# Optimization experiments

Measured on AMD Instinct MI355X. Metric: run time of the kernel, lower is better.

## Reference

```python
import jax, jax.numpy as jnp
import numpy as np

MUL = 32            # multiplicity of each irrep
N_NODES = 16384
N_EDGES = 262144
AVG_NEIGH = 16.0
N_SPECIES = 4
RADIAL_DIM = 8
INV_SQRT3 = 0.5773502691896258  # normalized CG coeff for 1o x 1o -> 0e (dot)


def setup_inputs() -> dict:
    key = jax.random.key(0)
    ks = jax.random.split(key, 14)
    f32 = jnp.float32
    return {
        "node_features": jax.random.normal(ks[0], (N_NODES, 4 * MUL), dtype=f32),
        "edge_sh": jax.random.normal(ks[1], (N_EDGES, 4), dtype=f32),
        "radial_embedding": jax.random.uniform(ks[2], (N_EDGES, RADIAL_DIM), dtype=f32),
        "W_up_s": jax.random.normal(ks[3], (MUL, MUL), dtype=f32),
        "W_up_v": jax.random.normal(ks[4], (MUL, MUL), dtype=f32),
        "W_r1": jax.random.normal(ks[5], (RADIAL_DIM, RADIAL_DIM), dtype=f32),
        "W_r2": jax.random.normal(ks[6], (RADIAL_DIM, 4 * MUL), dtype=f32),
        "W_dn_s": jax.random.normal(ks[7], (2 * MUL, 2 * MUL), dtype=f32),
        "W_dn_v": jax.random.normal(ks[8], (2 * MUL, MUL), dtype=f32),
        "W_sk_s": jax.random.normal(ks[9], (N_SPECIES, MUL, 2 * MUL), dtype=f32),
        "W_sk_v": jax.random.normal(ks[10], (N_SPECIES, MUL, MUL), dtype=f32),
        "senders": jax.random.randint(ks[11], (N_EDGES,), 0, N_NODES),
        "receivers": jax.random.randint(ks[12], (N_EDGES,), 0, N_NODES),
        "node_species": jax.random.randint(ks[13], (N_NODES,), 0, N_SPECIES),
    }


def reference(node_features, edge_sh, radial_embedding, W_up_s, W_up_v,
              W_r1, W_r2, W_dn_s, W_dn_v, W_sk_s, W_sk_v,
              senders, receivers, node_species):
    n = node_features.shape[0]
    # irreps layout: 32x0e (first MUL cols) + 32x1o (next 3*MUL cols)
    s = node_features[:, :MUL]                      # [N, mul]     0e
    v = node_features[:, MUL:].reshape(n, MUL, 3)   # [N, mul, 3]  1o

    # linear_up: per-irrep channel mixing, 1/sqrt(fan_in) normalization
    s1 = (s @ W_up_s) * (MUL ** -0.5)
    v1 = jnp.einsum('nmi,mk->nki', v, W_up_v) * (MUL ** -0.5)

    # gather sender features per edge
    ss = s1[senders]              # [E, mul]
    vs = v1[senders]              # [E, mul, 3]
    yv = edge_sh[:, 1:4]          # 1o part of edge spherical harmonics (0e part dropped in TP)

    # Clebsch-Gordan tensor product, filtered to output irreps {0e, 1o}:
    #   0e x 1o -> 1o ;  1o x 1o -> 0e (dot, coeff 1/sqrt(3)); cross(1e) & 2e dropped
    m_v_tp = ss[:, :, None] * yv[:, None, :]                 # [E, mul, 3]
    m_s_tp = jnp.einsum('emi,ei->em', vs, yv) * INV_SQRT3    # [E, mul]

    # radial MLP -> one scalar weight per irrep instance of the message
    h = jax.nn.silu((radial_embedding @ W_r1) * (RADIAL_DIM ** -0.5))
    w = (h @ W_r2) * (RADIAL_DIM ** -0.5)                    # [E, 4*mul]
    w_ss, w_vs, w_vt, w_st = jnp.split(w, 4, axis=1)

    # message = concat(self-features, tensor-product paths), radially weighted
    m_s = jnp.concatenate([ss * w_ss, m_s_tp * w_st], axis=1)                          # [E, 2*mul]
    m_v = jnp.concatenate([vs * w_vs[:, :, None], m_v_tp * w_vt[:, :, None]], axis=1)  # [E, 2*mul, 3]

    # scatter-add into receiver nodes, divide by sqrt(avg_num_neighbours)
    inv = AVG_NEIGH ** -0.5
    S = jax.ops.segment_sum(m_s, receivers, num_segments=n) * inv                     # [N, 2*mul]
    V = jax.ops.segment_sum(m_v.reshape(m_v.shape[0], -1), receivers,
                            num_segments=n).reshape(n, 2 * MUL, 3) * inv              # [N, 2*mul, 3]

    # linear_down to gate irreps: MUL 0e features + MUL gate scalars, MUL 1o vectors
    g_s = (S @ W_dn_s) * ((2 * MUL) ** -0.5)                                          # [N, 2*mul]
    g_v = jnp.einsum('nmi,mk->nki', V, W_dn_v) * ((2 * MUL) ** -0.5)                  # [N, mul, 3]

    # species-indexed skip connection from the original node features
    sk_s = jnp.einsum('nm,nmk->nk', s, W_sk_s[node_species]) * (MUL ** -0.5)
    sk_v = jnp.einsum('nmi,nmk->nki', v, W_sk_v[node_species]) * (MUL ** -0.5)
    g_s = 0.5 * (g_s + sk_s)
    g_v = 0.5 * (g_v + sk_v)

    # gate nonlinearity: silu on even scalars, silu(gates) multiplies each 1o vector
    feat_s = jax.nn.silu(g_s[:, :MUL])
    gates = jax.nn.silu(g_s[:, MUL:])
    out_v = g_v * gates[:, :, None]
    return jnp.concatenate([feat_s, out_v.reshape(n, 3 * MUL)], axis=1)  # [N, 4*mul]
```

## Files before the change

### kernel.cpp

```cpp
#include <hip/hip_runtime.h>
#include <hip/hip_bf16.h>
#include <hip/hip_fp16.h>

#define N_NODES 16384
#define N_EDGES 262144
#define MUL 32
#define REC_CAP (N_EDGES + 3 * N_NODES + 16)

#if defined(__has_builtin)
#if __has_builtin(__builtin_amdgcn_fdot2)
#define HAS_FDOT2 1
#endif
#endif

typedef _Float16 h2_t __attribute__((ext_vector_type(2)));

__device__ __forceinline__ float silu_f(float x) {
    return x / (1.0f + __expf(-x));
}
__device__ __forceinline__ __half2 i2h2(int v) { return __builtin_bit_cast(__half2, v); }
__device__ __forceinline__ int h22i(__half2 v) { return __builtin_bit_cast(int, v); }
__device__ __forceinline__ h2_t mkh2(float a, float b) {
    h2_t r; r[0] = (_Float16)a; r[1] = (_Float16)b; return r;
}
__device__ __forceinline__ float dot2(int hbits, h2_t w, float acc) {
#ifdef HAS_FDOT2
    return __builtin_amdgcn_fdot2(__builtin_bit_cast(h2_t, hbits), w, acc, false);
#else
    float2 h = __half22float2(i2h2(hbits));
    return acc + h.x * (float)w[0] + h.y * (float)w[1];
#endif
}

__global__ void k_up(const float* __restrict__ nf,
                     const float* __restrict__ Wus,
                     const float* __restrict__ Wuv,
                     __half* __restrict__ up_h,
                     const int* __restrict__ recv,
                     int* __restrict__ counts,
                     int* __restrict__ rank) {
    __shared__ float sh[2][128];
    int node0 = blockIdx.x * 2;
    int t = threadIdx.x;
    if (t < 32) {
        int e = blockIdx.x * 32 + t;
        rank[e] = atomicAdd(&counts[recv[e]], 1);
    }
    sh[t >> 7][t & 127] = nf[(size_t)node0 * 128 + t];
    __syncthreads();
    int local = t >> 7;
    int c = t & 127;
    int m = c >> 2, comp = c & 3;
    const float* row = sh[local];
    float acc = 0.f;
    if (comp == 0) {
        #pragma unroll
        for (int k = 0; k < 32; ++k) acc += row[k] * Wus[k * 32 + m];
    } else {
        int i = comp - 1;
        #pragma unroll
        for (int k = 0; k < 32; ++k) acc += row[32 + k * 3 + i] * Wuv[k * 32 + m];
    }
    up_h[(size_t)(node0 + local) * 128 + c] = __float2half(acc * 0.17677669529663687f);
}

__global__ void k_scan(const int* __restrict__ counts,
                       int* __restrict__ starts,
                       const float* __restrict__ Wdns,
                       const float* __restrict__ Wdnv,
                       const float* __restrict__ Wsks,
                       const float* __restrict__ Wskv,
                       float4* __restrict__ pk_dn,
                       float4* __restrict__ pk_sk) {
    __shared__ int wtot[16];
    __shared__ int woff[16];
    int t = threadIdx.x;
    int lane = t & 63, wid = t >> 6;
    const int4* cp = (const int4*)(counts + t * 16);
    int4 c0 = cp[0], c1 = cp[1], c2 = cp[2], c3 = cp[3];
    int cs[16] = {c0.x,c0.y,c0.z,c0.w,c1.x,c1.y,c1.z,c1.w,
                  c2.x,c2.y,c2.z,c2.w,c3.x,c3.y,c3.z,c3.w};
    int mysum = 0;
    #pragma unroll
    for (int i = 0; i < 16; ++i) {
        cs[i] = (cs[i] + 3) & ~3;
        mysum += cs[i];
    }
    int incl = mysum;
    #pragma unroll
    for (int off = 1; off < 64; off <<= 1) {
        int y = __shfl_up(incl, off, 64);
        if (lane >= off) incl += y;
    }
    if (lane == 63) wtot[wid] = incl;

    for (int i = t; i < 2048; i += 1024) {
        int mm = i >> 5, m = i & 31;
        pk_dn[i] = make_float4(Wdns[mm * 64 + m], Wdns[mm * 64 + 32 + m],
                               Wdnv[mm * 32 + m], 0.f);
    }
    for (int i = t; i < 4096; i += 1024) {
        int sp = i >> 10, mm = (i >> 5) & 31, m = i & 31;
        pk_sk[i] = make_float4(Wsks[sp * 2048 + mm * 64 + m],
                               Wsks[sp * 2048 + mm * 64 + 32 + m],
                               Wskv[sp * 1024 + mm * 32 + m], 0.f);
    }

    __syncthreads();
    if (t == 0) {
        int run = 0;
        #pragma unroll
        for (int w = 0; w < 16; ++w) { woff[w] = run; run += wtot[w]; }
    }
    __syncthreads();
    int run = woff[wid] + (incl - mysum);
    #pragma unroll
    for (int i = 0; i < 16; ++i) {
        starts[t * 16 + i] = run;
        run += cs[i];
    }
    if (t == 1023) starts[N_NODES] = run;
}

__global__ void k_edges(const float* __restrict__ rad,
                        const float* __restrict__ Wr1,
                        const int* __restrict__ recv,
                        const int* __restrict__ senders,
                        const float* __restrict__ esh,
                        const int* __restrict__ starts,
                        const int* __restrict__ counts,
                        const int* __restrict__ rank,
                        int4* __restrict__ records) {
    int e = blockIdx.x * blockDim.x + threadIdx.x;
    const int4 z = make_int4(0, 0, 0, 0);

    if (e < N_NODES) {
        int st = starts[e] + counts[e];
        int en = starts[e + 1];
        for (int p = st; p < en; ++p) {
            records[2 * (size_t)p] = z;
            records[2 * (size_t)p + 1] = z;
        }
    }
    if (e < 16) {
        int total = starts[N_NODES];
        records[2 * (size_t)(total + e)] = z;
        records[2 * (size_t)(total + e) + 1] = z;
    }

    const float4* rp = (const float4*)(rad + (size_t)e * 8);
    float4 a = rp[0], b = rp[1];
    float r[8] = {a.x, a.y, a.z, a.w, b.x, b.y, b.z, b.w};
    float h[8];
    #pragma unroll
    for (int j = 0; j < 8; ++j) {
        float acc = 0.f;
        #pragma unroll
        for (int k = 0; k < 8; ++k) acc += r[k] * Wr1[k * 8 + j];
        h[j] = silu_f(acc * 0.35355339059327373f);
    }
    float4 ey = *(const float4*)(esh + (size_t)e * 4);
    int snd = senders[e];
    int rc = recv[e];
    int pos = starts[rc] + rank[e];
    int4 meta;
    meta.x = snd;
    meta.y = h22i(__floats2half2_rn(ey.y, ey.z));
    meta.z = h22i(__floats2half2_rn(ey.w, 0.f));
    meta.w = 0;
    int4 hp;
    hp.x = h22i(__floats2half2_rn(h[0], h[1]));
    hp.y = h22i(__floats2half2_rn(h[2], h[3]));
    hp.z = h22i(__floats2half2_rn(h[4], h[5]));
    hp.w = h22i(__floats2half2_rn(h[6], h[7]));
    records[2 * (size_t)pos] = meta;
    records[2 * (size_t)pos + 1] = hp;
}

struct Acc {
    float S0, S1, Vv0, Vv1, Vv2, Vt0, Vt1, Vt2;
};
__device__ __forceinline__ void edge_accum(int4 meta, int4 hp, int2 q,
                                           const h2_t* __restrict__ w2a,
                                           const h2_t* __restrict__ w2b,
                                           const h2_t* __restrict__ w2c,
                                           const h2_t* __restrict__ w2d,
                                           Acc& A) {
    float wss = dot2(hp.x, w2a[0], dot2(hp.y, w2a[1], dot2(hp.z, w2a[2], dot2(hp.w, w2a[3], 0.f))));
    float wvs = dot2(hp.x, w2b[0], dot2(hp.y, w2b[1], dot2(hp.z, w2b[2], dot2(hp.w, w2b[3], 0.f))));
    float wvt = dot2(hp.x, w2c[0], dot2(hp.y, w2c[1], dot2(hp.z, w2c[2], dot2(hp.w, w2c[3], 0.f))));
    float wst = dot2(hp.x, w2d[0], dot2(hp.y, w2d[1], dot2(hp.z, w2d[2], dot2(hp.w, w2d[3], 0.f))));

    float2 y01 = __half22float2(i2h2(meta.y));
    float2 y2p = __half22float2(i2h2(meta.z));
    float y0 = y01.x, y1 = y01.y, y2 = y2p.x;
    float2 sv0 = __half22float2(i2h2(q.x));
    float2 v12 = __half22float2(i2h2(q.y));
    float ss = sv0.x, v0 = sv0.y, v1v = v12.x, v2 = v12.y;
    float dot = v0 * y0 + v1v * y1 + v2 * y2;
    A.S0 += ss * wss;
    A.S1 += dot * wst;
    A.Vv0 += v0 * wvs; A.Vv1 += v1v * wvs; A.Vv2 += v2 * wvs;
    float tv = ss * wvt;
    A.Vt0 += tv * y0; A.Vt1 += tv * y1; A.Vt2 += tv * y2;
}

__launch_bounds__(256, 4)
__global__ void k_gather(const __half* __restrict__ up_h,
                         const float* __restrict__ nf,
                         const int4* __restrict__ records,
                         const float* __restrict__ Wr2,
                         const int* __restrict__ starts,
                         const float4* __restrict__ pk_dn,
                         const float4* __restrict__ pk_sk,
                         const int* __restrict__ species,
                         float* __restrict__ out) {
    __shared__ float4 agg4[4][64];
    __shared__ float4 sk4[4][32];

    int tid = threadIdx.x;
    int w = tid >> 6;
    int lane = tid & 63;
    int sub = lane >> 5;
    int m = lane & 31;
    int node = blockIdx.x * 4 + w;

    int s0 = starts[node], s1 = starts[node + 1];

    int ta = s0 + sub;
    const int4* rp;
    rp = records + 2 * (size_t)ta;        int4 c0 = rp[0], c1 = rp[1];
    rp = records + 2 * (size_t)(ta + 2);  int4 d0 = rp[0], d1 = rp[1];

    if (lane < 32) {
        const float* src = nf + (size_t)node * 128;
        float s = src[lane];
        float a0 = src[32 + 3 * lane + 0];
        float a1 = src[32 + 3 * lane + 1];
        float a2 = src[32 + 3 * lane + 2];
        sk4[w][lane] = make_float4(s, a0, a1, a2);
    }

    int2 qa = *(const int2*)(up_h + (size_t)c0.x * 128 + m * 4);
    int2 qb = *(const int2*)(up_h + (size_t)d0.x * 128 + m * 4);

    rp = records + 2 * (size_t)(ta + 4);  int4 n0 = rp[0], n1 = rp[1];
    rp = records + 2 * (size_t)(ta + 6);  int4 e0 = rp[0], e1 = rp[1];

    const float s8 = 0.35355339059327373f;
    const float s8s3 = 0.35355339059327373f * 0.5773502691896258f;
    h2_t w2a[4], w2b[4], w2c[4], w2d[4];
    #pragma unroll
    for (int j4 = 0; j4 < 4; ++j4) {
        int j = 2 * j4;
        w2a[j4] = mkh2(Wr2[j * 128 + m] * s8,        Wr2[(j + 1) * 128 + m] * s8);
        w2b[j4] = mkh2(Wr2[j * 128 + 32 + m] * s8,   Wr2[(j + 1) * 128 + 32 + m] * s8);
        w2c[j4] = mkh2(Wr2[j * 128 + 64 + m] * s8,   Wr2[(j + 1) * 128 + 64 + m] * s8);
        w2d[j4] = mkh2(Wr2[j * 128 + 96 + m] * s8s3, Wr2[(j + 1) * 128 + 96 + m] * s8s3);
    }

    Acc A = {0.f,0.f,0.f,0.f,0.f,0.f,0.f,0.f};
    Acc B = {0.f,0.f,0.f,0.f,0.f,0.f,0.f,0.f};

    #pragma unroll 1
    for (int t0 = s0; t0 < s1; t0 += 4) {
        int2 qna = *(const int2*)(up_h + (size_t)n0.x * 128 + m * 4);
        int2 qnb = *(const int2*)(up_h + (size_t)e0.x * 128 + m * 4);

        int t2 = t0 + 8 + sub;
        rp = records + 2 * (size_t)t2;        int4 p0 = rp[0], p1 = rp[1];
        rp = records + 2 * (size_t)(t2 + 2);  int4 r0 = rp[0], r1 = rp[1];

        edge_accum(c0, c1, qa, w2a, w2b, w2c, w2d, A);
        edge_accum(d0, d1, qb, w2a, w2b, w2c, w2d, B);

        c0 = n0; c1 = n1; d0 = e0; d1 = e1;
        qa = qna; qb = qnb;
        n0 = p0; n1 = p1; e0 = r0; e1 = r1;
    }

    float accS0 = A.S0 + B.S0, accS1 = A.S1 + B.S1;
    float accVv0 = A.Vv0 + B.Vv0, accVv1 = A.Vv1 + B.Vv1, accVv2 = A.Vv2 + B.Vv2;
    float accVt0 = A.Vt0 + B.Vt0, accVt1 = A.Vt1 + B.Vt1, accVt2 = A.Vt2 + B.Vt2;

    accS0 += __shfl_xor(accS0, 32, 64);
    accS1 += __shfl_xor(accS1, 32, 64);
    accVv0 += __shfl_xor(accVv0, 32, 64);
    accVv1 += __shfl_xor(accVv1, 32, 64);
    accVv2 += __shfl_xor(accVv2, 32, 64);
    accVt0 += __shfl_xor(accVt0, 32, 64);
    accVt1 += __shfl_xor(accVt1, 32, 64);
    accVt2 += __shfl_xor(accVt2, 32, 64);

    const float inv_neigh = 0.25f;
    if (sub == 0) {
        agg4[w][m]      = make_float4(accS0 * inv_neigh, accVv0 * inv_neigh,
                                      accVv1 * inv_neigh, accVv2 * inv_neigh);
        agg4[w][32 + m] = make_float4(accS1 * inv_neigh, accVt0 * inv_neigh,
                                      accVt1 * inv_neigh, accVt2 * inv_neigh);
    }

    int sp = species[node];

    float gsa = 0.f, gsb = 0.f, gv0 = 0.f, gv1 = 0.f, gv2 = 0.f;
    {
        const float4* agp = agg4[w];
        int mm0 = sub * 32;
        #pragma unroll 4
        for (int k = 0; k < 32; ++k) {
            int mm = mm0 + k;
            float4 sv = agp[mm];
            float4 wq = pk_dn[mm * 32 + m];
            gsa += sv.x * wq.x;
            gsb += sv.x * wq.y;
            gv0 += sv.y * wq.z;
            gv1 += sv.z * wq.z;
            gv2 += sv.w * wq.z;
        }
    }
    float ska = 0.f, skb = 0.f, skv0 = 0.f, skv1 = 0.f, skv2 = 0.f;
    {
        const float4* pks = pk_sk + (size_t)sp * 1024;
        int mm0 = sub * 16;
        #pragma unroll 4
        for (int k = 0; k < 16; ++k) {
            int mm = mm0 + k;
            float4 sv = sk4[w][mm];
            float4 wq = pks[mm * 32 + m];
            ska += sv.x * wq.x;
            skb += sv.x * wq.y;
            skv0 += sv.y * wq.z;
            skv1 += sv.z * wq.z;
            skv2 += sv.w * wq.z;
        }
    }
    gsa += __shfl_xor(gsa, 32, 64);
    gsb += __shfl_xor(gsb, 32, 64);
    gv0 += __shfl_xor(gv0, 32, 64);
    gv1 += __shfl_xor(gv1, 32, 64);
    gv2 += __shfl_xor(gv2, 32, 64);
    ska += __shfl_xor(ska, 32, 64);
    skb += __shfl_xor(skb, 32, 64);
    skv0 += __shfl_xor(skv0, 32, 64);
    skv1 += __shfl_xor(skv1, 32, 64);
    skv2 += __shfl_xor(skv2, 32, 64);

    if (sub == 0) {
        const float inv8 = 0.125f;
        const float isq32 = 0.17677669529663687f;
        float a  = 0.5f * (gsa * inv8 + ska * isq32);
        float b  = 0.5f * (gsb * inv8 + skb * isq32);
        float o0 = 0.5f * (gv0 * inv8 + skv0 * isq32);
        float o1 = 0.5f * (gv1 * inv8 + skv1 * isq32);
        float o2 = 0.5f * (gv2 * inv8 + skv2 * isq32);

        float feat = silu_f(a);
        float gate = silu_f(b);
        float* o = out + (size_t)node * 128;
        o[m] = feat;
        o[32 + 3 * m + 0] = o0 * gate;
        o[32 + 3 * m + 1] = o1 * gate;
        o[32 + 3 * m + 2] = o2 * gate;
    }
}

extern "C" void kernel_launch(void* const* d_in, const int* in_sizes, int n_in,
                              void* d_out, int out_size, void* d_ws, size_t ws_size,
                              hipStream_t stream) {
    const float* nf   = (const float*)d_in[0];
    const float* esh  = (const float*)d_in[1];
    const float* rad  = (const float*)d_in[2];
    const float* Wus  = (const float*)d_in[3];
    const float* Wuv  = (const float*)d_in[4];
    const float* Wr1  = (const float*)d_in[5];
    const float* Wr2  = (const float*)d_in[6];
    const float* Wdns = (const float*)d_in[7];
    const float* Wdnv = (const float*)d_in[8];
    const float* Wsks = (const float*)d_in[9];
    const float* Wskv = (const float*)d_in[10];
    const int* senders   = (const int*)d_in[11];
    const int* receivers = (const int*)d_in[12];
    const int* species   = (const int*)d_in[13];
    float* out = (float*)d_out;

    char* ws = (char*)d_ws;
    __half* up_h   = (__half*)(ws);
    int4* records  = (int4*)(ws + (4u << 20));
    int* counts    = (int*)(ws + (14u << 20));
    int* starts    = (int*)(ws + (14u << 20) + 65536);
    int* rank      = (int*)(ws + (15u << 20));
    float4* pk_dn  = (float4*)(ws + (16u << 20));
    float4* pk_sk  = (float4*)(ws + (16u << 20) + 32768);

    hipMemsetAsync(counts, 0, 65536, stream);
    k_up<<<N_NODES / 2, 256, 0, stream>>>(nf, Wus, Wuv, up_h, receivers, counts, rank);
    k_scan<<<1, 1024, 0, stream>>>(counts, starts, Wdns, Wdnv, Wsks, Wskv, pk_dn, pk_sk);
    k_edges<<<N_EDGES / 256, 256, 0, stream>>>(rad, Wr1, receivers, senders, esh,
                                               starts, counts, rank, records);
    k_gather<<<N_NODES / 4, 256, 0, stream>>>(up_h, nf, records, Wr2, starts,
                                              pk_dn, pk_sk, species, out);
}
```

Before: 176.1 us.

## Compute edge records in edge order and scatter only indices into CSR

Edge records (radial MLP hidden, packed spherical harmonics, sender) are now computed in k_up and stored in edge order. The sorting pass only scatters 4-byte edge indices instead of 32-byte records, and padding slots point to a zeroed sentinel record. Weight packing moves from the single-block scan kernel into the scatter kernel to shorten the serial scan. The gather kernel now reads records through an extra level of indirection with random access, which adds latency and loses the sequential record reads it had before.

```diff
diff --git a/kernel.cpp b/kernel.cpp
--- a/kernel.cpp
+++ b/kernel.cpp
@@ -5,7 +5,7 @@
 #define N_NODES 16384
 #define N_EDGES 262144
 #define MUL 32
-#define REC_CAP (N_EDGES + 3 * N_NODES + 16)
+#define IDX_CAP (N_EDGES + 3 * N_NODES + 16)
 
 #if defined(__has_builtin)
 #if __has_builtin(__builtin_amdgcn_fdot2)
@@ -37,14 +37,49 @@
                      const float* __restrict__ Wuv,
                      __half* __restrict__ up_h,
                      const int* __restrict__ recv,
+                     const int* __restrict__ senders,
+                     const float* __restrict__ esh,
+                     const float* __restrict__ rad,
+                     const float* __restrict__ Wr1,
                      int* __restrict__ counts,
-                     int* __restrict__ rank) {
+                     int* __restrict__ rank,
+                     int4* __restrict__ rec_e) {
     __shared__ float sh[2][128];
     int node0 = blockIdx.x * 2;
     int t = threadIdx.x;
     if (t < 32) {
         int e = blockIdx.x * 32 + t;
-        rank[e] = atomicAdd(&counts[recv[e]], 1);
+        int rc = recv[e];
+        rank[e] = atomicAdd(&counts[rc], 1);
+        const float4* rp4 = (const float4*)(rad + (size_t)e * 8);
+        float4 a = rp4[0], b = rp4[1];
+        float r[8] = {a.x, a.y, a.z, a.w, b.x, b.y, b.z, b.w};
+        float h[8];
+        #pragma unroll
+        for (int j = 0; j < 8; ++j) {
+            float acc = 0.f;
+            #pragma unroll
+            for (int k = 0; k < 8; ++k) acc += r[k] * Wr1[k * 8 + j];
+            h[j] = silu_f(acc * 0.35355339059327373f);
+        }
+        float4 ey = *(const float4*)(esh + (size_t)e * 4);
+        int4 meta;
+        meta.x = senders[e];
+        meta.y = h22i(__floats2half2_rn(ey.y, ey.z));
+        meta.z = h22i(__floats2half2_rn(ey.w, 0.f));
+        meta.w = 0;
+        int4 hp;
+        hp.x = h22i(__floats2half2_rn(h[0], h[1]));
+        hp.y = h22i(__floats2half2_rn(h[2], h[3]));
+        hp.z = h22i(__floats2half2_rn(h[4], h[5]));
+        hp.w = h22i(__floats2half2_rn(h[6], h[7]));
+        rec_e[2 * (size_t)e] = meta;
+        rec_e[2 * (size_t)e + 1] = hp;
+    }
+    if (blockIdx.x == 0 && t == 32) {
+        const int4 z = make_int4(0, 0, 0, 0);
+        rec_e[2 * (size_t)N_EDGES] = z;
+        rec_e[2 * (size_t)N_EDGES + 1] = z;
     }
     sh[t >> 7][t & 127] = nf[(size_t)node0 * 128 + t];
     __syncthreads();
@@ -65,13 +100,7 @@
 }
 
 __global__ void k_scan(const int* __restrict__ counts,
-                       int* __restrict__ starts,
-                       const float* __restrict__ Wdns,
-                       const float* __restrict__ Wdnv,
-                       const float* __restrict__ Wsks,
-                       const float* __restrict__ Wskv,
-                       float4* __restrict__ pk_dn,
-                       float4* __restrict__ pk_sk) {
+                       int* __restrict__ starts) {
     __shared__ int wtot[16];
     __shared__ int woff[16];
     int t = threadIdx.x;
@@ -93,19 +122,6 @@
         if (lane >= off) incl += y;
     }
     if (lane == 63) wtot[wid] = incl;
-
-    for (int i = t; i < 2048; i += 1024) {
-        int mm = i >> 5, m = i & 31;
-        pk_dn[i] = make_float4(Wdns[mm * 64 + m], Wdns[mm * 64 + 32 + m],
-                               Wdnv[mm * 32 + m], 0.f);
-    }
-    for (int i = t; i < 4096; i += 1024) {
-        int sp = i >> 10, mm = (i >> 5) & 31, m = i & 31;
-        pk_sk[i] = make_float4(Wsks[sp * 2048 + mm * 64 + m],
-                               Wsks[sp * 2048 + mm * 64 + 32 + m],
-                               Wskv[sp * 1024 + mm * 32 + m], 0.f);
-    }
-
     __syncthreads();
     if (t == 0) {
         int run = 0;
@@ -122,59 +138,40 @@
     if (t == 1023) starts[N_NODES] = run;
 }
 
-__global__ void k_edges(const float* __restrict__ rad,
-                        const float* __restrict__ Wr1,
-                        const int* __restrict__ recv,
-                        const int* __restrict__ senders,
-                        const float* __restrict__ esh,
-                        const int* __restrict__ starts,
-                        const int* __restrict__ counts,
-                        const int* __restrict__ rank,
-                        int4* __restrict__ records) {
+__global__ void k_scatter(const int* __restrict__ recv,
+                          const int* __restrict__ starts,
+                          const int* __restrict__ counts,
+                          const int* __restrict__ rank,
+                          int* __restrict__ edge_idx,
+                          const float* __restrict__ Wdns,
+                          const float* __restrict__ Wdnv,
+                          const float* __restrict__ Wsks,
+                          const float* __restrict__ Wskv,
+                          float4* __restrict__ pk_dn,
+                          float4* __restrict__ pk_sk) {
     int e = blockIdx.x * blockDim.x + threadIdx.x;
-    const int4 z = make_int4(0, 0, 0, 0);
+
+    if (e < 2048) {
+        int mm = e >> 5, m = e & 31;
+        pk_dn[e] = make_float4(Wdns[mm * 64 + m], Wdns[mm * 64 + 32 + m],
+                               Wdnv[mm * 32 + m], 0.f);
+    } else if (e < 2048 + 4096) {
+        int j = e - 2048;
+        int sp = j >> 10, mm = (j >> 5) & 31, m = j & 31;
+        pk_sk[j] = make_float4(Wsks[sp * 2048 + mm * 64 + m],
+                               Wsks[sp * 2048 + mm * 64 + 32 + m],
+                               Wskv[sp * 1024 + mm * 32 + m], 0.f);
+    }
 
     if (e < N_NODES) {
         int st = starts[e] + counts[e];
         int en = starts[e + 1];
-        for (int p = st; p < en; ++p) {
-            records[2 * (size_t)p] = z;
-            records[2 * (size_t)p + 1] = z;
-        }
-    }
-    if (e < 16) {
-        int total = starts[N_NODES];
-        records[2 * (size_t)(total + e)] = z;
-        records[2 * (size_t)(total + e) + 1] = z;
-    }
-
-    const float4* rp = (const float4*)(rad + (size_t)e * 8);
-    float4 a = rp[0], b = rp[1];
-    float r[8] = {a.x, a.y, a.z, a.w, b.x, b.y, b.z, b.w};
-    float h[8];
-    #pragma unroll
-    for (int j = 0; j < 8; ++j) {
-        float acc = 0.f;
-        #pragma unroll
-        for (int k = 0; k < 8; ++k) acc += r[k] * Wr1[k * 8 + j];
-        h[j] = silu_f(acc * 0.35355339059327373f);
-    }
-    float4 ey = *(const float4*)(esh + (size_t)e * 4);
-    int snd = senders[e];
-    int rc = recv[e];
-    int pos = starts[rc] + rank[e];
-    int4 meta;
-    meta.x = snd;
-    meta.y = h22i(__floats2half2_rn(ey.y, ey.z));
-    meta.z = h22i(__floats2half2_rn(ey.w, 0.f));
-    meta.w = 0;
-    int4 hp;
-    hp.x = h22i(__floats2half2_rn(h[0], h[1]));
-    hp.y = h22i(__floats2half2_rn(h[2], h[3]));
-    hp.z = h22i(__floats2half2_rn(h[4], h[5]));
-    hp.w = h22i(__floats2half2_rn(h[6], h[7]));
-    records[2 * (size_t)pos] = meta;
-    records[2 * (size_t)pos + 1] = hp;
+        for (int p = st; p < en; ++p) edge_idx[p] = N_EDGES;
+    }
+    if (e < 16) edge_idx[starts[N_NODES] + e] = N_EDGES;
+
+    int pos = starts[recv[e]] + rank[e];
+    edge_idx[pos] = e;
 }
 
 struct Acc {
@@ -208,7 +205,8 @@
 __launch_bounds__(256, 4)
 __global__ void k_gather(const __half* __restrict__ up_h,
                          const float* __restrict__ nf,
-                         const int4* __restrict__ records,
+                         const int* __restrict__ edge_idx,
+                         const int4* __restrict__ rec_e,
                          const float* __restrict__ Wr2,
                          const int* __restrict__ starts,
                          const float4* __restrict__ pk_dn,
@@ -226,11 +224,11 @@
     int node = blockIdx.x * 4 + w;
 
     int s0 = starts[node], s1 = starts[node + 1];
-
-    int ta = s0 + sub;
-    const int4* rp;
-    rp = records + 2 * (size_t)ta;        int4 c0 = rp[0], c1 = rp[1];
-    rp = records + 2 * (size_t)(ta + 2);  int4 d0 = rp[0], d1 = rp[1];
+    int base = s0 + 2 * sub;
+
+    int2 eid0 = *(const int2*)(edge_idx + base);
+    int2 eid1 = *(const int2*)(edge_idx + base + 4);
+    int2 eid2 = *(const int2*)(edge_idx + base + 8);
 
     if (lane < 32) {
         const float* src = nf + (size_t)node * 128;
@@ -241,11 +239,14 @@
         sk4[w][lane] = make_float4(s, a0, a1, a2);
     }
 
-    int2 qa = *(const int2*)(up_h + (size_t)c0.x * 128 + m * 4);
-    int2 qb = *(const int2*)(up_h + (size_t)d0.x * 128 + m * 4);
-
-    rp = records + 2 * (size_t)(ta + 4);  int4 n0 = rp[0], n1 = rp[1];
-    rp = records + 2 * (size_t)(ta + 6);  int4 e0 = rp[0], e1 = rp[1];
+    const int4* rp;
+    rp = rec_e + 2 * (size_t)eid0.x;  int4 ca0 = rp[0], ca1 = rp[1];
+    rp = rec_e + 2 * (size_t)eid0.y;  int4 cb0 = rp[0], cb1 = rp[1];
+    rp = rec_e + 2 * (size_t)eid1.x;  int4 na0 = rp[0], na1 = rp[1];
+    rp = rec_e + 2 * (size_t)eid1.y;  int4 nb0 = rp[0], nb1 = rp[1];
+
+    int2 qa = *(const int2*)(up_h + (size_t)ca0.x * 128 + m * 4);
+    int2 qb = *(const int2*)(up_h + (size_t)cb0.x * 128 + m * 4);
 
     const float s8 = 0.35355339059327373f;
     const float s8s3 = 0.35355339059327373f * 0.5773502691896258f;
@@ -263,20 +264,22 @@
     Acc B = {0.f,0.f,0.f,0.f,0.f,0.f,0.f,0.f};
 
     #pragma unroll 1
-    for (int t0 = s0; t0 < s1; t0 += 4) {
-        int2 qna = *(const int2*)(up_h + (size_t)n0.x * 128 + m * 4);
-        int2 qnb = *(const int2*)(up_h + (size_t)e0.x * 128 + m * 4);
-
-        int t2 = t0 + 8 + sub;
-        rp = records + 2 * (size_t)t2;        int4 p0 = rp[0], p1 = rp[1];
-        rp = records + 2 * (size_t)(t2 + 2);  int4 r0 = rp[0], r1 = rp[1];
-
-        edge_accum(c0, c1, qa, w2a, w2b, w2c, w2d, A);
-        edge_accum(d0, d1, qb, w2a, w2b, w2c, w2d, B);
-
-        c0 = n0; c1 = n1; d0 = e0; d1 = e1;
+    for (int t0 = s0; t0 < s1; t0 += 4, base += 4) {
+        int2 qna = *(const int2*)(up_h + (size_t)na0.x * 128 + m * 4);
+        int2 qnb = *(const int2*)(up_h + (size_t)nb0.x * 128 + m * 4);
+
+        rp = rec_e + 2 * (size_t)eid2.x;  int4 pa0 = rp[0], pa1 = rp[1];
+        rp = rec_e + 2 * (size_t)eid2.y;  int4 pb0 = rp[0], pb1 = rp[1];
+
+        int2 eid3 = *(const int2*)(edge_idx + base + 12);
+
+        edge_accum(ca0, ca1, qa, w2a, w2b, w2c, w2d, A);
+        edge_accum(cb0, cb1, qb, w2a, w2b, w2c, w2d, B);
+
+        ca0 = na0; ca1 = na1; cb0 = nb0; cb1 = nb1;
+        na0 = pa0; na1 = pa1; nb0 = pb0; nb1 = pb1;
         qa = qna; qb = qnb;
-        n0 = p0; n1 = p1; e0 = r0; e1 = r1;
+        eid2 = eid3;
     }
 
     float accS0 = A.S0 + B.S0, accS1 = A.S1 + B.S1;
@@ -385,18 +388,21 @@
 
     char* ws = (char*)d_ws;
     __half* up_h   = (__half*)(ws);
-    int4* records  = (int4*)(ws + (4u << 20));
-    int* counts    = (int*)(ws + (14u << 20));
-    int* starts    = (int*)(ws + (14u << 20) + 65536);
-    int* rank      = (int*)(ws + (15u << 20));
-    float4* pk_dn  = (float4*)(ws + (16u << 20));
-    float4* pk_sk  = (float4*)(ws + (16u << 20) + 32768);
+    int4* rec_e    = (int4*)(ws + (4u << 20));
+    int* edge_idx  = (int*)(ws + (13u << 20));
+    int* counts    = (int*)(ws + (15u << 20));
+    int* starts    = (int*)(ws + (15u << 20) + 65536);
+    int* rank      = (int*)(ws + (15u << 20) + 131076);
+    float4* pk_dn  = (float4*)(ws + (17u << 20));
+    float4* pk_sk  = (float4*)(ws + (17u << 20) + 32768);
 
     hipMemsetAsync(counts, 0, 65536, stream);
-    k_up<<<N_NODES / 2, 256, 0, stream>>>(nf, Wus, Wuv, up_h, receivers, counts, rank);
-    k_scan<<<1, 1024, 0, stream>>>(counts, starts, Wdns, Wdnv, Wsks, Wskv, pk_dn, pk_sk);
-    k_edges<<<N_EDGES / 256, 256, 0, stream>>>(rad, Wr1, receivers, senders, esh,
-                                               starts, counts, rank, records);
-    k_gather<<<N_NODES / 4, 256, 0, stream>>>(up_h, nf, records, Wr2, starts,
+    k_up<<<N_NODES / 2, 256, 0, stream>>>(nf, Wus, Wuv, up_h, receivers, senders,
+                                          esh, rad, Wr1, counts, rank, rec_e);
+    k_scan<<<1, 1024, 0, stream>>>(counts, starts);
+    k_scatter<<<N_EDGES / 256, 256, 0, stream>>>(receivers, starts, counts, rank,
+                                                 edge_idx, Wdns, Wdnv, Wsks, Wskv,
+                                                 pk_dn, pk_sk);
+    k_gather<<<N_NODES / 4, 256, 0, stream>>>(up_h, nf, edge_idx, rec_e, Wr2, starts,
                                               pk_dn, pk_sk, species, out);
 }
```

Result: no change. 176.9 us (+0.4%).

## Fuse all stages into one cooperative persistent kernel with grid syncs

Applied to the files above, without the earlier changes.

Replaces the memset plus four kernel launches with a single cooperative kernel that runs counting, linear_up, scan, record building and the gather/output stages, separated by grid-wide syncs. Each block now owns a contiguous slice of nodes and edges and loops over them. The aim is to remove launch gaps and the serial single-block scan launch. In exchange it adds grid-sync barriers, and the scan still runs on one block of 256 threads while the rest of the grid waits. Occupancy is also limited to a grid sized for cooperative residency.

```diff
diff --git a/kernel.cpp b/kernel.cpp
--- a/kernel.cpp
+++ b/kernel.cpp
@@ -1,10 +1,11 @@
 #include <hip/hip_runtime.h>
-#include <hip/hip_bf16.h>
 #include <hip/hip_fp16.h>
+#include <hip/hip_cooperative_groups.h>
+
+namespace cg = cooperative_groups;
 
 #define N_NODES 16384
 #define N_EDGES 262144
-#define MUL 32
 #define REC_CAP (N_EDGES + 3 * N_NODES + 16)
 
 #if defined(__has_builtin)
@@ -30,151 +31,6 @@
     float2 h = __half22float2(i2h2(hbits));
     return acc + h.x * (float)w[0] + h.y * (float)w[1];
 #endif
-}
-
-__global__ void k_up(const float* __restrict__ nf,
-                     const float* __restrict__ Wus,
-                     const float* __restrict__ Wuv,
-                     __half* __restrict__ up_h,
-                     const int* __restrict__ recv,
-                     int* __restrict__ counts,
-                     int* __restrict__ rank) {
-    __shared__ float sh[2][128];
-    int node0 = blockIdx.x * 2;
-    int t = threadIdx.x;
-    if (t < 32) {
-        int e = blockIdx.x * 32 + t;
-        rank[e] = atomicAdd(&counts[recv[e]], 1);
-    }
-    sh[t >> 7][t & 127] = nf[(size_t)node0 * 128 + t];
-    __syncthreads();
-    int local = t >> 7;
-    int c = t & 127;
-    int m = c >> 2, comp = c & 3;
-    const float* row = sh[local];
-    float acc = 0.f;
-    if (comp == 0) {
-        #pragma unroll
-        for (int k = 0; k < 32; ++k) acc += row[k] * Wus[k * 32 + m];
-    } else {
-        int i = comp - 1;
-        #pragma unroll
-        for (int k = 0; k < 32; ++k) acc += row[32 + k * 3 + i] * Wuv[k * 32 + m];
-    }
-    up_h[(size_t)(node0 + local) * 128 + c] = __float2half(acc * 0.17677669529663687f);
-}
-
-__global__ void k_scan(const int* __restrict__ counts,
-                       int* __restrict__ starts,
-                       const float* __restrict__ Wdns,
-                       const float* __restrict__ Wdnv,
-                       const float* __restrict__ Wsks,
-                       const float* __restrict__ Wskv,
-                       float4* __restrict__ pk_dn,
-                       float4* __restrict__ pk_sk) {
-    __shared__ int wtot[16];
-    __shared__ int woff[16];
-    int t = threadIdx.x;
-    int lane = t & 63, wid = t >> 6;
-    const int4* cp = (const int4*)(counts + t * 16);
-    int4 c0 = cp[0], c1 = cp[1], c2 = cp[2], c3 = cp[3];
-    int cs[16] = {c0.x,c0.y,c0.z,c0.w,c1.x,c1.y,c1.z,c1.w,
-                  c2.x,c2.y,c2.z,c2.w,c3.x,c3.y,c3.z,c3.w};
-    int mysum = 0;
-    #pragma unroll
-    for (int i = 0; i < 16; ++i) {
-        cs[i] = (cs[i] + 3) & ~3;
-        mysum += cs[i];
-    }
-    int incl = mysum;
-    #pragma unroll
-    for (int off = 1; off < 64; off <<= 1) {
-        int y = __shfl_up(incl, off, 64);
-        if (lane >= off) incl += y;
-    }
-    if (lane == 63) wtot[wid] = incl;
-
-    for (int i = t; i < 2048; i += 1024) {
-        int mm = i >> 5, m = i & 31;
-        pk_dn[i] = make_float4(Wdns[mm * 64 + m], Wdns[mm * 64 + 32 + m],
-                               Wdnv[mm * 32 + m], 0.f);
-    }
-    for (int i = t; i < 4096; i += 1024) {
-        int sp = i >> 10, mm = (i >> 5) & 31, m = i & 31;
-        pk_sk[i] = make_float4(Wsks[sp * 2048 + mm * 64 + m],
-                               Wsks[sp * 2048 + mm * 64 + 32 + m],
-                               Wskv[sp * 1024 + mm * 32 + m], 0.f);
-    }
-
-    __syncthreads();
-    if (t == 0) {
-        int run = 0;
-        #pragma unroll
-        for (int w = 0; w < 16; ++w) { woff[w] = run; run += wtot[w]; }
-    }
-    __syncthreads();
-    int run = woff[wid] + (incl - mysum);
-    #pragma unroll
-    for (int i = 0; i < 16; ++i) {
-        starts[t * 16 + i] = run;
-        run += cs[i];
-    }
-    if (t == 1023) starts[N_NODES] = run;
-}
-
-__global__ void k_edges(const float* __restrict__ rad,
-                        const float* __restrict__ Wr1,
-                        const int* __restrict__ recv,
-                        const int* __restrict__ senders,
-                        const float* __restrict__ esh,
-                        const int* __restrict__ starts,
-                        const int* __restrict__ counts,
-                        const int* __restrict__ rank,
-                        int4* __restrict__ records) {
-    int e = blockIdx.x * blockDim.x + threadIdx.x;
-    const int4 z = make_int4(0, 0, 0, 0);
-
-    if (e < N_NODES) {
-        int st = starts[e] + counts[e];
-        int en = starts[e + 1];
-        for (int p = st; p < en; ++p) {
-            records[2 * (size_t)p] = z;
-            records[2 * (size_t)p + 1] = z;
-        }
-    }
-    if (e < 16) {
-        int total = starts[N_NODES];
-        records[2 * (size_t)(total + e)] = z;
-        records[2 * (size_t)(total + e) + 1] = z;
-    }
-
-    const float4* rp = (const float4*)(rad + (size_t)e * 8);
-    float4 a = rp[0], b = rp[1];
-    float r[8] = {a.x, a.y, a.z, a.w, b.x, b.y, b.z, b.w};
-    float h[8];
-    #pragma unroll
-    for (int j = 0; j < 8; ++j) {
-        float acc = 0.f;
-        #pragma unroll
-        for (int k = 0; k < 8; ++k) acc += r[k] * Wr1[k * 8 + j];
-        h[j] = silu_f(acc * 0.35355339059327373f);
-    }
-    float4 ey = *(const float4*)(esh + (size_t)e * 4);
-    int snd = senders[e];
-    int rc = recv[e];
-    int pos = starts[rc] + rank[e];
-    int4 meta;
-    meta.x = snd;
-    meta.y = h22i(__floats2half2_rn(ey.y, ey.z));
-    meta.z = h22i(__floats2half2_rn(ey.w, 0.f));
-    meta.w = 0;
-    int4 hp;
-    hp.x = h22i(__floats2half2_rn(h[0], h[1]));
-    hp.y = h22i(__floats2half2_rn(h[2], h[3]));
-    hp.z = h22i(__floats2half2_rn(h[4], h[5]));
-    hp.w = h22i(__floats2half2_rn(h[6], h[7]));
-    records[2 * (size_t)pos] = meta;
-    records[2 * (size_t)pos + 1] = hp;
 }
 
 struct Acc {
@@ -206,46 +62,152 @@
 }
 
 __launch_bounds__(256, 4)
-__global__ void k_gather(const __half* __restrict__ up_h,
-                         const float* __restrict__ nf,
-                         const int4* __restrict__ records,
-                         const float* __restrict__ Wr2,
-                         const int* __restrict__ starts,
-                         const float4* __restrict__ pk_dn,
-                         const float4* __restrict__ pk_sk,
-                         const int* __restrict__ species,
-                         float* __restrict__ out) {
+__global__ void mega(const float* __restrict__ nf, const float* __restrict__ esh,
+                     const float* __restrict__ rad, const float* __restrict__ Wus,
+                     const float* __restrict__ Wuv, const float* __restrict__ Wr1,
+                     const float* __restrict__ Wr2, const float* __restrict__ Wdns,
+                     const float* __restrict__ Wdnv, const float* __restrict__ Wsks,
+                     const float* __restrict__ Wskv, const int* __restrict__ senders,
+                     const int* __restrict__ recv, const int* __restrict__ species,
+                     float* __restrict__ out, __half* __restrict__ up_h,
+                     int4* __restrict__ records, int* __restrict__ counts,
+                     int* __restrict__ starts, int* __restrict__ rank,
+                     float4* __restrict__ pk_dn, float4* __restrict__ pk_sk) {
+    cg::grid_group gg = cg::this_grid();
+    const int b = blockIdx.x, t = threadIdx.x;
+    const int nblocks = gridDim.x;
+    const int nb = N_NODES / nblocks;
+    const int eb = N_EDGES / nblocks;
+
+    __shared__ float sh[2][128];
     __shared__ float4 agg4[4][64];
     __shared__ float4 sk4[4][32];
-
-    int tid = threadIdx.x;
-    int w = tid >> 6;
-    int lane = tid & 63;
-    int sub = lane >> 5;
-    int m = lane & 31;
-    int node = blockIdx.x * 4 + w;
-
-    int s0 = starts[node], s1 = starts[node + 1];
-
-    int ta = s0 + sub;
-    const int4* rp;
-    rp = records + 2 * (size_t)ta;        int4 c0 = rp[0], c1 = rp[1];
-    rp = records + 2 * (size_t)(ta + 2);  int4 d0 = rp[0], d1 = rp[1];
-
-    if (lane < 32) {
-        const float* src = nf + (size_t)node * 128;
-        float s = src[lane];
-        float a0 = src[32 + 3 * lane + 0];
-        float a1 = src[32 + 3 * lane + 1];
-        float a2 = src[32 + 3 * lane + 2];
-        sk4[w][lane] = make_float4(s, a0, a1, a2);
-    }
-
-    int2 qa = *(const int2*)(up_h + (size_t)c0.x * 128 + m * 4);
-    int2 qb = *(const int2*)(up_h + (size_t)d0.x * 128 + m * 4);
-
-    rp = records + 2 * (size_t)(ta + 4);  int4 n0 = rp[0], n1 = rp[1];
-    rp = records + 2 * (size_t)(ta + 6);  int4 e0 = rp[0], e1 = rp[1];
+    __shared__ int wtot[4];
+    __shared__ int woff[4];
+
+    if (t < nb) counts[b * nb + t] = 0;
+    {
+        int gid = b * 256 + t;
+        if (gid < 2048) {
+            int mm = gid >> 5, m0 = gid & 31;
+            pk_dn[gid] = make_float4(Wdns[mm * 64 + m0], Wdns[mm * 64 + 32 + m0],
+                                     Wdnv[mm * 32 + m0], 0.f);
+        } else if (gid < 6144) {
+            int j = gid - 2048;
+            int sp = j >> 10, mm = (j >> 5) & 31, m0 = j & 31;
+            pk_sk[j] = make_float4(Wsks[sp * 2048 + mm * 64 + m0],
+                                   Wsks[sp * 2048 + mm * 64 + 32 + m0],
+                                   Wskv[sp * 1024 + mm * 32 + m0], 0.f);
+        }
+    }
+    gg.sync();
+
+    for (int k = 0; k < eb; k += 256) {
+        int e = b * eb + k + t;
+        rank[e] = atomicAdd(&counts[recv[e]], 1);
+    }
+    for (int it = 0; it < nb / 2; ++it) {
+        int node0 = b * nb + it * 2;
+        sh[t >> 7][t & 127] = nf[(size_t)node0 * 128 + t];
+        __syncthreads();
+        int local = t >> 7, c = t & 127, mq = c >> 2, comp = c & 3;
+        const float* row = sh[local];
+        float acc = 0.f;
+        if (comp == 0) {
+            #pragma unroll
+            for (int k2 = 0; k2 < 32; ++k2) acc += row[k2] * Wus[k2 * 32 + mq];
+        } else {
+            int i = comp - 1;
+            #pragma unroll
+            for (int k2 = 0; k2 < 32; ++k2) acc += row[32 + k2 * 3 + i] * Wuv[k2 * 32 + mq];
+        }
+        up_h[(size_t)(node0 + local) * 128 + c] = __float2half(acc * 0.17677669529663687f);
+        __syncthreads();
+    }
+    gg.sync();
+
+    if (b == 0) {
+        int base = t * 64;
+        int tot = 0;
+        for (int i = 0; i < 64; i += 4) {
+            int4 c4 = *(const int4*)(counts + base + i);
+            tot += ((c4.x + 3) & ~3) + ((c4.y + 3) & ~3) +
+                   ((c4.z + 3) & ~3) + ((c4.w + 3) & ~3);
+        }
+        int lane2 = t & 63, wid = t >> 6;
+        int incl = tot;
+        #pragma unroll
+        for (int off = 1; off < 64; off <<= 1) {
+            int y = __shfl_up(incl, off, 64);
+            if (lane2 >= off) incl += y;
+        }
+        if (lane2 == 63) wtot[wid] = incl;
+        __syncthreads();
+        if (t == 0) {
+            int run = 0;
+            #pragma unroll
+            for (int q = 0; q < 4; ++q) { woff[q] = run; run += wtot[q]; }
+        }
+        __syncthreads();
+        int run = woff[wid] + (incl - tot);
+        for (int i = 0; i < 64; i += 4) {
+            int4 c4 = *(const int4*)(counts + base + i);
+            starts[base + i]     = run; run += (c4.x + 3) & ~3;
+            starts[base + i + 1] = run; run += (c4.y + 3) & ~3;
+            starts[base + i + 2] = run; run += (c4.z + 3) & ~3;
+            starts[base + i + 3] = run; run += (c4.w + 3) & ~3;
+        }
+        if (t == 255) starts[N_NODES] = run;
+    }
+    gg.sync();
+
+    if (t < nb) {
+        int n = b * nb + t;
+        int st = starts[n] + counts[n];
+        int en = starts[n + 1];
+        const int4 z = make_int4(0, 0, 0, 0);
+        for (int p = st; p < en; ++p) {
+            records[2 * (size_t)p] = z;
+            records[2 * (size_t)p + 1] = z;
+        }
+    }
+    if (b == 0 && t < 16) {
+        const int4 z = make_int4(0, 0, 0, 0);
+        int total = starts[N_NODES];
+        records[2 * (size_t)(total + t)] = z;
+        records[2 * (size_t)(total + t) + 1] = z;
+    }
+    for (int k = 0; k < eb; k += 256) {
+        int e = b * eb + k + t;
+        const float4* rp4 = (const float4*)(rad + (size_t)e * 8);
+        float4 a4 = rp4[0], b4 = rp4[1];
+        float r[8] = {a4.x, a4.y, a4.z, a4.w, b4.x, b4.y, b4.z, b4.w};
+        float h[8];
+        #pragma unroll
+        for (int j = 0; j < 8; ++j) {
+            float acc = 0.f;
+            #pragma unroll
+            for (int k2 = 0; k2 < 8; ++k2) acc += r[k2] * Wr1[k2 * 8 + j];
+            h[j] = silu_f(acc * 0.35355339059327373f);
+        }
+        float4 ey = *(const float4*)(esh + (size_t)e * 4);
+        int pos = starts[recv[e]] + rank[e];
+        int4 meta;
+        meta.x = senders[e];
+        meta.y = h22i(__floats2half2_rn(ey.y, ey.z));
+        meta.z = h22i(__floats2half2_rn(ey.w, 0.f));
+        meta.w = 0;
+        int4 hp;
+        hp.x = h22i(__floats2half2_rn(h[0], h[1]));
+        hp.y = h22i(__floats2half2_rn(h[2], h[3]));
+        hp.z = h22i(__floats2half2_rn(h[4], h[5]));
+        hp.w = h22i(__floats2half2_rn(h[6], h[7]));
+        records[2 * (size_t)pos] = meta;
+        records[2 * (size_t)pos + 1] = hp;
+    }
+    gg.sync();
+
+    const int w = t >> 6, lane = t & 63, sub = lane >> 5, m = lane & 31;
 
     const float s8 = 0.35355339059327373f;
     const float s8s3 = 0.35355339059327373f * 0.5773502691896258f;
@@ -259,108 +221,130 @@
         w2d[j4] = mkh2(Wr2[j * 128 + 96 + m] * s8s3, Wr2[(j + 1) * 128 + 96 + m] * s8s3);
     }
 
-    Acc A = {0.f,0.f,0.f,0.f,0.f,0.f,0.f,0.f};
-    Acc B = {0.f,0.f,0.f,0.f,0.f,0.f,0.f,0.f};
-
-    #pragma unroll 1
-    for (int t0 = s0; t0 < s1; t0 += 4) {
-        int2 qna = *(const int2*)(up_h + (size_t)n0.x * 128 + m * 4);
-        int2 qnb = *(const int2*)(up_h + (size_t)e0.x * 128 + m * 4);
-
-        int t2 = t0 + 8 + sub;
-        rp = records + 2 * (size_t)t2;        int4 p0 = rp[0], p1 = rp[1];
-        rp = records + 2 * (size_t)(t2 + 2);  int4 r0 = rp[0], r1 = rp[1];
-
-        edge_accum(c0, c1, qa, w2a, w2b, w2c, w2d, A);
-        edge_accum(d0, d1, qb, w2a, w2b, w2c, w2d, B);
-
-        c0 = n0; c1 = n1; d0 = e0; d1 = e1;
-        qa = qna; qb = qnb;
-        n0 = p0; n1 = p1; e0 = r0; e1 = r1;
-    }
-
-    float accS0 = A.S0 + B.S0, accS1 = A.S1 + B.S1;
-    float accVv0 = A.Vv0 + B.Vv0, accVv1 = A.Vv1 + B.Vv1, accVv2 = A.Vv2 + B.Vv2;
-    float accVt0 = A.Vt0 + B.Vt0, accVt1 = A.Vt1 + B.Vt1, accVt2 = A.Vt2 + B.Vt2;
-
-    accS0 += __shfl_xor(accS0, 32, 64);
-    accS1 += __shfl_xor(accS1, 32, 64);
-    accVv0 += __shfl_xor(accVv0, 32, 64);
-    accVv1 += __shfl_xor(accVv1, 32, 64);
-    accVv2 += __shfl_xor(accVv2, 32, 64);
-    accVt0 += __shfl_xor(accVt0, 32, 64);
-    accVt1 += __shfl_xor(accVt1, 32, 64);
-    accVt2 += __shfl_xor(accVt2, 32, 64);
-
-    const float inv_neigh = 0.25f;
-    if (sub == 0) {
-        agg4[w][m]      = make_float4(accS0 * inv_neigh, accVv0 * inv_neigh,
-                                      accVv1 * inv_neigh, accVv2 * inv_neigh);
-        agg4[w][32 + m] = make_float4(accS1 * inv_neigh, accVt0 * inv_neigh,
-                                      accVt1 * inv_neigh, accVt2 * inv_neigh);
-    }
-
-    int sp = species[node];
-
-    float gsa = 0.f, gsb = 0.f, gv0 = 0.f, gv1 = 0.f, gv2 = 0.f;
-    {
-        const float4* agp = agg4[w];
-        int mm0 = sub * 32;
-        #pragma unroll 4
-        for (int k = 0; k < 32; ++k) {
-            int mm = mm0 + k;
-            float4 sv = agp[mm];
-            float4 wq = pk_dn[mm * 32 + m];
-            gsa += sv.x * wq.x;
-            gsb += sv.x * wq.y;
-            gv0 += sv.y * wq.z;
-            gv1 += sv.z * wq.z;
-            gv2 += sv.w * wq.z;
-        }
-    }
-    float ska = 0.f, skb = 0.f, skv0 = 0.f, skv1 = 0.f, skv2 = 0.f;
-    {
-        const float4* pks = pk_sk + (size_t)sp * 1024;
-        int mm0 = sub * 16;
-        #pragma unroll 4
-        for (int k = 0; k < 16; ++k) {
-            int mm = mm0 + k;
-            float4 sv = sk4[w][mm];
-            float4 wq = pks[mm * 32 + m];
-            ska += sv.x * wq.x;
-            skb += sv.x * wq.y;
-            skv0 += sv.y * wq.z;
-            skv1 += sv.z * wq.z;
-            skv2 += sv.w * wq.z;
-        }
-    }
-    gsa += __shfl_xor(gsa, 32, 64);
-    gsb += __shfl_xor(gsb, 32, 64);
-    gv0 += __shfl_xor(gv0, 32, 64);
-    gv1 += __shfl_xor(gv1, 32, 64);
-    gv2 += __shfl_xor(gv2, 32, 64);
-    ska += __shfl_xor(ska, 32, 64);
-    skb += __shfl_xor(skb, 32, 64);
-    skv0 += __shfl_xor(skv0, 32, 64);
-    skv1 += __shfl_xor(skv1, 32, 64);
-    skv2 += __shfl_xor(skv2, 32, 64);
-
-    if (sub == 0) {
-        const float inv8 = 0.125f;
-        const float isq32 = 0.17677669529663687f;
-        float a  = 0.5f * (gsa * inv8 + ska * isq32);
-        float b  = 0.5f * (gsb * inv8 + skb * isq32);
-        float o0 = 0.5f * (gv0 * inv8 + skv0 * isq32);
-        float o1 = 0.5f * (gv1 * inv8 + skv1 * isq32);
-        float o2 = 0.5f * (gv2 * inv8 + skv2 * isq32);
-
-        float feat = silu_f(a);
-        float gate = silu_f(b);
-        float* o = out + (size_t)node * 128;
-        o[m] = feat;
-        o[32 + 3 * m + 0] = o0 * gate;
-        o[32 + 3 * m + 1] = o1 * gate;
-        o[32 + 3 * m + 2] = o2 * gate;
+    for (int chunk = 0; chunk < nb / 4; ++chunk) {
+        int node = b * nb + chunk * 4 + w;
+        int s0 = starts[node], s1 = starts[node + 1];
+
+        int ta = s0 + sub;
+        const int4* rp;
+        rp = records + 2 * (size_t)ta;        int4 c0 = rp[0], c1 = rp[1];
+        rp = records + 2 * (size_t)(ta + 2);  int4 d0 = rp[0], d1 = rp[1];
+
+        if (lane < 32) {
+            const float* src = nf + (size_t)node * 128;
+            sk4[w][lane] = make_float4(src[lane], src[32 + 3 * lane],
+                                       src[33 + 3 * lane], src[34 + 3 * lane]);
+        }
+
+        int2 qa = *(const int2*)(up_h + (size_t)c0.x * 128 + m * 4);
+        int2 qb = *(const int2*)(up_h + (size_t)d0.x * 128 + m * 4);
+
+        rp = records + 2 * (size_t)(ta + 4);  int4 n0 = rp[0], n1 = rp[1];
+        rp = records + 2 * (size_t)(ta + 6);  int4 e0 = rp[0], e1 = rp[1];
+
+        Acc A = {0.f,0.f,0.f,0.f,0.f,0.f,0.f,0.f};
+        Acc B = {0.f,0.f,0.f,0.f,0.f,0.f,0.f,0.f};
+
+        #pragma unroll 1
+        for (int t0 = s0; t0 < s1; t0 += 4) {
+            int2 qna = *(const int2*)(up_h + (size_t)n0.x * 128 + m * 4);
+            int2 qnb = *(const int2*)(up_h + (size_t)e0.x * 128 + m * 4);
+
+            int t2 = t0 + 8 + sub;
+            rp = records + 2 * (size_t)t2;        int4 p0 = rp[0], p1 = rp[1];
+            rp = records + 2 * (size_t)(t2 + 2);  int4 r0 = rp[0], r1 = rp[1];
+
+            edge_accum(c0, c1, qa, w2a, w2b, w2c, w2d, A);
+            edge_accum(d0, d1, qb, w2a, w2b, w2c, w2d, B);
+
+            c0 = n0; c1 = n1; d0 = e0; d1 = e1;
+            qa = qna; qb = qnb;
+            n0 = p0; n1 = p1; e0 = r0; e1 = r1;
+        }
+
+        float accS0 = A.S0 + B.S0, accS1 = A.S1 + B.S1;
+        float accVv0 = A.Vv0 + B.Vv0, accVv1 = A.Vv1 + B.Vv1, accVv2 = A.Vv2 + B.Vv2;
+        float accVt0 = A.Vt0 + B.Vt0, accVt1 = A.Vt1 + B.Vt1, accVt2 = A.Vt2 + B.Vt2;
+
+        accS0 += __shfl_xor(accS0, 32, 64);
+        accS1 += __shfl_xor(accS1, 32, 64);
+        accVv0 += __shfl_xor(accVv0, 32, 64);
+        accVv1 += __shfl_xor(accVv1, 32, 64);
+        accVv2 += __shfl_xor(accVv2, 32, 64);
+        accVt0 += __shfl_xor(accVt0, 32, 64);
+        accVt1 += __shfl_xor(accVt1, 32, 64);
+        accVt2 += __shfl_xor(accVt2, 32, 64);
+
+        const float inv_neigh = 0.25f;
+        if (sub == 0) {
+            agg4[w][m]      = make_float4(accS0 * inv_neigh, accVv0 * inv_neigh,
+                                          accVv1 * inv_neigh, accVv2 * inv_neigh);
+            agg4[w][32 + m] = make_float4(accS1 * inv_neigh, accVt0 * inv_neigh,
+                                          accVt1 * inv_neigh, accVt2 * inv_neigh);
+        }
+
+        int sp = species[node];
+
+        float gsa = 0.f, gsb = 0.f, gv0 = 0.f, gv1 = 0.f, gv2 = 0.f;
+        {
+            const float4* agp = agg4[w];
+            int mm0 = sub * 32;
+            #pragma unroll 4
+            for (int k = 0; k < 32; ++k) {
+                int mm = mm0 + k;
+                float4 sv = agp[mm];
+                float4 wq = pk_dn[mm * 32 + m];
+                gsa += sv.x * wq.x;
+                gsb += sv.x * wq.y;
+                gv0 += sv.y * wq.z;
+                gv1 += sv.z * wq.z;
+                gv2 += sv.w * wq.z;
+            }
+        }
+        float ska = 0.f, skb = 0.f, skv0 = 0.f, skv1 = 0.f, skv2 = 0.f;
+        {
+            const float4* pks = pk_sk + (size_t)sp * 1024;
+            int mm0 = sub * 16;
+            #pragma unroll 4
+            for (int k = 0; k < 16; ++k) {
+                int mm = mm0 + k;
+                float4 sv = sk4[w][mm];
+                float4 wq = pks[mm * 32 + m];
+                ska += sv.x * wq.x;
+                skb += sv.x * wq.y;
+                skv0 += sv.y * wq.z;
+                skv1 += sv.z * wq.z;
+                skv2 += sv.w * wq.z;
+            }
+        }
+        gsa += __shfl_xor(gsa, 32, 64);
+        gsb += __shfl_xor(gsb, 32, 64);
+        gv0 += __shfl_xor(gv0, 32, 64);
+        gv1 += __shfl_xor(gv1, 32, 64);
+        gv2 += __shfl_xor(gv2, 32, 64);
+        ska += __shfl_xor(ska, 32, 64);
+        skb += __shfl_xor(skb, 32, 64);
+        skv0 += __shfl_xor(skv0, 32, 64);
+        skv1 += __shfl_xor(skv1, 32, 64);
+        skv2 += __shfl_xor(skv2, 32, 64);
+
+        if (sub == 0) {
+            const float inv8 = 0.125f;
+            const float isq32 = 0.17677669529663687f;
+            float a  = 0.5f * (gsa * inv8 + ska * isq32);
+            float bb = 0.5f * (gsb * inv8 + skb * isq32);
+            float o0 = 0.5f * (gv0 * inv8 + skv0 * isq32);
+            float o1 = 0.5f * (gv1 * inv8 + skv1 * isq32);
+            float o2 = 0.5f * (gv2 * inv8 + skv2 * isq32);
+
+            float feat = silu_f(a);
+            float gate = silu_f(bb);
+            float* o = out + (size_t)node * 128;
+            o[m] = feat;
+            o[32 + 3 * m + 0] = o0 * gate;
+            o[32 + 3 * m + 1] = o1 * gate;
+            o[32 + 3 * m + 2] = o2 * gate;
+        }
     }
 }
 
@@ -392,11 +376,20 @@
     float4* pk_dn  = (float4*)(ws + (16u << 20));
     float4* pk_sk  = (float4*)(ws + (16u << 20) + 32768);
 
-    hipMemsetAsync(counts, 0, 65536, stream);
-    k_up<<<N_NODES / 2, 256, 0, stream>>>(nf, Wus, Wuv, up_h, receivers, counts, rank);
-    k_scan<<<1, 1024, 0, stream>>>(counts, starts, Wdns, Wdnv, Wsks, Wskv, pk_dn, pk_sk);
-    k_edges<<<N_EDGES / 256, 256, 0, stream>>>(rad, Wr1, receivers, senders, esh,
-                                               starts, counts, rank, records);
-    k_gather<<<N_NODES / 4, 256, 0, stream>>>(up_h, nf, records, Wr2, starts,
-                                              pk_dn, pk_sk, species, out);
-}
+    int perCU = 0;
+    hipError_t qe = hipOccupancyMaxActiveBlocksPerMultiprocessor(&perCU, mega, 256, 0);
+    if (qe != hipSuccess || perCU <= 0) perCU = 4;
+    int maxBlocks = perCU * 256;
+    int grid = 1024;
+    if (maxBlocks < 1024) grid = 512;
+    if (maxBlocks < 512) grid = 256;
+
+    void* args[] = {
+        (void*)&nf, (void*)&esh, (void*)&rad, (void*)&Wus, (void*)&Wuv,
+        (void*)&Wr1, (void*)&Wr2, (void*)&Wdns, (void*)&Wdnv, (void*)&Wsks,
+        (void*)&Wskv, (void*)&senders, (void*)&receivers, (void*)&species,
+        (void*)&out, (void*)&up_h, (void*)&records, (void*)&counts,
+        (void*)&starts, (void*)&rank, (void*)&pk_dn, (void*)&pk_sk
+    };
+    hipLaunchCooperativeKernel((void*)mega, dim3(grid), dim3(256), args, 0, stream);
+}
```

New measurement: 437.3 us. 2.48x slower.
